# Kernel optimization log

Hardware: AMD Instinct MI355X
Metric: run time of the kernel (lower is better)

## Reference

```python
import jax, jax.numpy as jnp
import numpy as np

D_MODEL = 2048
NUM_EXPERTS = 64
TOP_K = 2
EPS = 1e-8


def setup_inputs() -> dict:
    key = jax.random.key(0)
    kx, kw = jax.random.split(key)
    x = jax.random.normal(kx, (32768, D_MODEL), dtype=jnp.float32)
    # nn.Linear(d_model, num_experts, bias=False) weight: [E, D], init std=0.02
    gate_w = jax.random.normal(kw, (NUM_EXPERTS, D_MODEL), dtype=jnp.float32) * 0.02
    expert_bias = jnp.zeros((NUM_EXPERTS,), dtype=jnp.float32)  # buffer, zeros at init
    return {"x": x, "gate_w": gate_w, "expert_bias": expert_bias}


def reference(x, gate_w, expert_bias):
    # logits = x @ W^T + bias  : [N, E]
    logits = jnp.einsum("nd,ed->ne", x, gate_w) + expert_bias
    routing_probs = jax.nn.softmax(logits, axis=-1)
    # top-k over experts, then renormalize selected weights
    routing_weights, selected_experts = jax.lax.top_k(routing_probs, TOP_K)
    routing_weights = routing_weights / (
        jnp.sum(routing_weights, axis=-1, keepdims=True) + EPS
    )
    return routing_weights, selected_experts
```

## Files before the change

### kernel.cpp

```cpp
#include <hip/hip_runtime.h>
#include <math.h>

#define D_MODEL 2048
#define NEXP    64
#define NROWS   32768
#define BM      64
#define BK      16
#define PAD     4
#define LDX     (BM + PAD)

__global__ __launch_bounds__(256, 2) void router_kernel(
    const float* __restrict__ x,
    const float* __restrict__ gw,
    const float* __restrict__ bias,
    float* __restrict__ out)
{
    __shared__ alignas(16) float xs[BK][LDX];
    __shared__ alignas(16) float ws[BK][LDX];
    __shared__ float logits[BM][NEXP + 1];

    const int t  = threadIdx.x;
    const int b  = blockIdx.x;
    const int r0 = b * BM;

    const int rg  = t & 15;
    const int eg  = t >> 4;
    const int rg4 = rg * 4;
    const int eg4 = eg * 4;

    const int sr  = t >> 2;
    const int skq = t & 3;
    const float* xrow = x  + (size_t)(r0 + sr) * D_MODEL + skq * 4;
    const float* wrow = gw + (size_t)sr        * D_MODEL + skq * 4;

    float acc[4][4];
#pragma unroll
    for (int i = 0; i < 4; ++i)
#pragma unroll
        for (int j = 0; j < 4; ++j) acc[i][j] = 0.f;

    float4 xv = *(const float4*)(xrow);
    float4 wv = *(const float4*)(wrow);

    for (int k0 = 0; k0 < D_MODEL; k0 += BK) {
        __syncthreads();
        {
            const int kq4 = skq * 4;
            xs[kq4 + 0][sr] = xv.x; xs[kq4 + 1][sr] = xv.y;
            xs[kq4 + 2][sr] = xv.z; xs[kq4 + 3][sr] = xv.w;
            ws[kq4 + 0][sr] = wv.x; ws[kq4 + 1][sr] = wv.y;
            ws[kq4 + 2][sr] = wv.z; ws[kq4 + 3][sr] = wv.w;
        }
        __syncthreads();

        if (k0 + BK < D_MODEL) {
            xv = *(const float4*)(xrow + k0 + BK);
            wv = *(const float4*)(wrow + k0 + BK);
        }

#pragma unroll
        for (int k = 0; k < BK; ++k) {
            const float4 xq = *(const float4*)&xs[k][rg4];
            const float4 wq = *(const float4*)&ws[k][eg4];
            acc[0][0] = fmaf(xq.x, wq.x, acc[0][0]);
            acc[0][1] = fmaf(xq.x, wq.y, acc[0][1]);
            acc[0][2] = fmaf(xq.x, wq.z, acc[0][2]);
            acc[0][3] = fmaf(xq.x, wq.w, acc[0][3]);
            acc[1][0] = fmaf(xq.y, wq.x, acc[1][0]);
            acc[1][1] = fmaf(xq.y, wq.y, acc[1][1]);
            acc[1][2] = fmaf(xq.y, wq.z, acc[1][2]);
            acc[1][3] = fmaf(xq.y, wq.w, acc[1][3]);
            acc[2][0] = fmaf(xq.z, wq.x, acc[2][0]);
            acc[2][1] = fmaf(xq.z, wq.y, acc[2][1]);
            acc[2][2] = fmaf(xq.z, wq.z, acc[2][2]);
            acc[2][3] = fmaf(xq.z, wq.w, acc[2][3]);
            acc[3][0] = fmaf(xq.w, wq.x, acc[3][0]);
            acc[3][1] = fmaf(xq.w, wq.y, acc[3][1]);
            acc[3][2] = fmaf(xq.w, wq.z, acc[3][2]);
            acc[3][3] = fmaf(xq.w, wq.w, acc[3][3]);
        }
    }

    __syncthreads();
#pragma unroll
    for (int i = 0; i < 4; ++i)
#pragma unroll
        for (int j = 0; j < 4; ++j)
            logits[rg4 + i][eg4 + j] = acc[i][j];
    __syncthreads();

    if (t < BM) {
        const int row = r0 + t;
        float m1 = -INFINITY, m2 = -INFINITY;
        int   e1 = 0, e2 = 0;
        for (int e = 0; e < NEXP; ++e) {
            const float l = logits[t][e] + bias[e];
            if (l > m1) { m2 = m1; e2 = e1; m1 = l; e1 = e; }
            else if (l > m2) { m2 = l; e2 = e; }
        }
        float z = 0.f;
        for (int e = 0; e < NEXP; ++e)
            z += expf(logits[t][e] + bias[e] - m1);
        const float p2    = expf(m2 - m1);
        const float denom = (1.f + p2) + 1e-8f * z;
        out[row * 2 + 0] = 1.f / denom;
        out[row * 2 + 1] = p2 / denom;
        float* oidx = out + 2 * NROWS;
        oidx[row * 2 + 0] = (float)e1;
        oidx[row * 2 + 1] = (float)e2;
    }
}

extern "C" void kernel_launch(void* const* d_in, const int* in_sizes, int n_in,
                              void* d_out, int out_size, void* d_ws, size_t ws_size,
                              hipStream_t stream) {
    const float* x    = (const float*)d_in[0];
    const float* gw   = (const float*)d_in[1];
    const float* bias = (const float*)d_in[2];
    float* out = (float*)d_out;
    (void)in_sizes; (void)n_in; (void)out_size; (void)d_ws; (void)ws_size;

    dim3 grid(NROWS / BM);
    dim3 block(256);
    router_kernel<<<grid, block, 0, stream>>>(x, gw, bias, out);
}
```

Measured before the change: 405.4 us.

## Restructure router GEMM to one row per thread with split-K waves

Replaces the shared-memory tiled outer-product GEMM with a scheme where each thread owns one token row and keeps all 64 expert logits in registers. The four waves of a block each cover a quarter of the K dimension, and their partial sums are reduced through shared memory before the top-2 softmax. Within a wave the gate weights are addressed uniformly, so they can come through scalar loads. This is meant to remove the per-tile LDS staging and the barriers inside the K loop. In exchange, x is read with strided per-lane access, register pressure rises, and the scalar-load bandwidth for the weights may become the limit.

New measurement: 825.9 us. 104% more time.

```diff
diff --git a/kernel.cpp b/kernel.cpp
--- a/kernel.cpp
+++ b/kernel.cpp
@@ -4,10 +4,10 @@
 #define D_MODEL 2048
 #define NEXP    64
 #define NROWS   32768
+#define SPLITS  4
+#define KSPL    (D_MODEL / SPLITS)
+#define GRP     16
 #define BM      64
-#define BK      16
-#define PAD     4
-#define LDX     (BM + PAD)
 
 __global__ __launch_bounds__(256, 2) void router_kernel(
     const float* __restrict__ x,
@@ -15,99 +15,70 @@
     const float* __restrict__ bias,
     float* __restrict__ out)
 {
-    __shared__ alignas(16) float xs[BK][LDX];
-    __shared__ alignas(16) float ws[BK][LDX];
-    __shared__ float logits[BM][NEXP + 1];
+    __shared__ float red[SPLITS][BM][NEXP + 1];
 
-    const int t  = threadIdx.x;
-    const int b  = blockIdx.x;
-    const int r0 = b * BM;
+    const int t    = threadIdx.x;
+    const int lane = t & 63;
+    const int wv   = t >> 6;
+    const int row  = blockIdx.x * BM + lane;
 
-    const int rg  = t & 15;
-    const int eg  = t >> 4;
-    const int rg4 = rg * 4;
-    const int eg4 = eg * 4;
+    const float* xp  = x  + (size_t)row * D_MODEL + wv * KSPL;
+    const float* wp0 = gw + wv * KSPL;
 
-    const int sr  = t >> 2;
-    const int skq = t & 3;
-    const float* xrow = x  + (size_t)(r0 + sr) * D_MODEL + skq * 4;
-    const float* wrow = gw + (size_t)sr        * D_MODEL + skq * 4;
+    float acc[NEXP];
+#pragma unroll
+    for (int e = 0; e < NEXP; ++e) acc[e] = 0.f;
 
-    float acc[4][4];
+    float4 xa[4], xb[4];
 #pragma unroll
-    for (int i = 0; i < 4; ++i)
+    for (int q = 0; q < 4; ++q) xa[q] = ((const float4*)xp)[q];
+
+    for (int g = 0; g < KSPL; g += GRP) {
+        if (g + GRP < KSPL) {
 #pragma unroll
-        for (int j = 0; j < 4; ++j) acc[i][j] = 0.f;
-
-    float4 xv = *(const float4*)(xrow);
-    float4 wv = *(const float4*)(wrow);
-
-    for (int k0 = 0; k0 < D_MODEL; k0 += BK) {
-        __syncthreads();
-        {
-            const int kq4 = skq * 4;
-            xs[kq4 + 0][sr] = xv.x; xs[kq4 + 1][sr] = xv.y;
-            xs[kq4 + 2][sr] = xv.z; xs[kq4 + 3][sr] = xv.w;
-            ws[kq4 + 0][sr] = wv.x; ws[kq4 + 1][sr] = wv.y;
-            ws[kq4 + 2][sr] = wv.z; ws[kq4 + 3][sr] = wv.w;
+            for (int q = 0; q < 4; ++q)
+                xb[q] = ((const float4*)(xp + g + GRP))[q];
         }
-        __syncthreads();
-
-        if (k0 + BK < D_MODEL) {
-            xv = *(const float4*)(xrow + k0 + BK);
-            wv = *(const float4*)(wrow + k0 + BK);
+        const float* xf = (const float*)xa;
+#pragma unroll
+        for (int e = 0; e < NEXP; ++e) {
+            const float* wp = wp0 + (size_t)e * D_MODEL + g;
+#pragma unroll
+            for (int j = 0; j < GRP; ++j)
+                acc[e] = fmaf(xf[j], wp[j], acc[e]);
         }
+#pragma unroll
+        for (int q = 0; q < 4; ++q) xa[q] = xb[q];
+    }
 
 #pragma unroll
-        for (int k = 0; k < BK; ++k) {
-            const float4 xq = *(const float4*)&xs[k][rg4];
-            const float4 wq = *(const float4*)&ws[k][eg4];
-            acc[0][0] = fmaf(xq.x, wq.x, acc[0][0]);
-            acc[0][1] = fmaf(xq.x, wq.y, acc[0][1]);
-            acc[0][2] = fmaf(xq.x, wq.z, acc[0][2]);
-            acc[0][3] = fmaf(xq.x, wq.w, acc[0][3]);
-            acc[1][0] = fmaf(xq.y, wq.x, acc[1][0]);
-            acc[1][1] = fmaf(xq.y, wq.y, acc[1][1]);
-            acc[1][2] = fmaf(xq.y, wq.z, acc[1][2]);
-            acc[1][3] = fmaf(xq.y, wq.w, acc[1][3]);
-            acc[2][0] = fmaf(xq.z, wq.x, acc[2][0]);
-            acc[2][1] = fmaf(xq.z, wq.y, acc[2][1]);
-            acc[2][2] = fmaf(xq.z, wq.z, acc[2][2]);
-            acc[2][3] = fmaf(xq.z, wq.w, acc[2][3]);
-            acc[3][0] = fmaf(xq.w, wq.x, acc[3][0]);
-            acc[3][1] = fmaf(xq.w, wq.y, acc[3][1]);
-            acc[3][2] = fmaf(xq.w, wq.z, acc[3][2]);
-            acc[3][3] = fmaf(xq.w, wq.w, acc[3][3]);
-        }
+    for (int e = 0; e < NEXP; e += 4) {
+        float4 v = make_float4(acc[e], acc[e + 1], acc[e + 2], acc[e + 3]);
+        *(float4*)&red[wv][lane][e] = v;
     }
-
-    __syncthreads();
-#pragma unroll
-    for (int i = 0; i < 4; ++i)
-#pragma unroll
-        for (int j = 0; j < 4; ++j)
-            logits[rg4 + i][eg4 + j] = acc[i][j];
     __syncthreads();
 
     if (t < BM) {
-        const int row = r0 + t;
+        const int grow = blockIdx.x * BM + t;
         float m1 = -INFINITY, m2 = -INFINITY;
         int   e1 = 0, e2 = 0;
         for (int e = 0; e < NEXP; ++e) {
-            const float l = logits[t][e] + bias[e];
+            float l = ((red[0][t][e] + red[1][t][e]) + red[2][t][e]) + red[3][t][e]
+                      + bias[e];
+            red[0][t][e] = l;
             if (l > m1) { m2 = m1; e2 = e1; m1 = l; e1 = e; }
             else if (l > m2) { m2 = l; e2 = e; }
         }
         float z = 0.f;
         for (int e = 0; e < NEXP; ++e)
-            z += expf(logits[t][e] + bias[e] - m1);
+            z += expf(red[0][t][e] - m1);
         const float p2    = expf(m2 - m1);
         const float denom = (1.f + p2) + 1e-8f * z;
-        out[row * 2 + 0] = 1.f / denom;
-        out[row * 2 + 1] = p2 / denom;
+        out[grow * 2 + 0] = 1.f / denom;
+        out[grow * 2 + 1] = p2 / denom;
         float* oidx = out + 2 * NROWS;
-        oidx[row * 2 + 0] = (float)e1;
-        oidx[row * 2 + 1] = (float)e2;
+        oidx[grow * 2 + 0] = (float)e1;
+        oidx[grow * 2 + 1] = (float)e2;
     }
 }
 
```
